# Optimization experiments

Hardware: AMD Instinct MI355X
Metric: run time of the kernel (lower is better)

The kernel has to match this reference:

```python
import jax, jax.numpy as jnp
import numpy as np
from jax import lax

K = 3
STRIDE = 1
PAD = 1
DIL = 1


def setup_inputs() -> dict:
    key = jax.random.key(0)
    k1, k2, k3 = jax.random.split(key, 3)
    B, C, H, W = 8, 128, 64, 64
    O = 128
    x = jax.random.normal(k1, (B, C, H, W), jnp.float32)
    # offset-predicting conv weights (small init -> small offsets, as in DCN practice)
    w_off = jax.random.normal(k2, (2 * K * K, C, K, K), jnp.float32) * 0.01
    b_off = jnp.zeros((2 * K * K,), jnp.float32)
    # deformable conv weight [O, Cin, K, K], bias=False in the source
    w = jax.random.normal(k3, (O, C, K, K), jnp.float32) * (1.0 / np.sqrt(C * K * K))
    return {"x": x, "w_off": w_off, "b_off": b_off, "w": w}


def _deform_conv(x, offset, w):
    # x: [B,C,H,W]; offset: [B, 2*K*K, Ho, Wo]; w: [O,C,K,K]
    B, C, H, W = x.shape
    Ho, Wo = offset.shape[2], offset.shape[3]
    K2 = K * K
    off = offset.reshape(B, K2, 2, Ho, Wo)
    oy, ox = off[:, :, 0], off[:, :, 1]            # [B,K2,Ho,Wo]
    ky = (jnp.arange(K2) // K).astype(jnp.float32)  # kernel row per tap
    kx = (jnp.arange(K2) % K).astype(jnp.float32)
    base_y = (jnp.arange(Ho) * STRIDE - PAD).astype(jnp.float32)
    base_x = (jnp.arange(Wo) * STRIDE - PAD).astype(jnp.float32)
    py = base_y[None, None, :, None] + ky[None, :, None, None] * DIL + oy
    px = base_x[None, None, None, :] + kx[None, :, None, None] * DIL + ox

    y0 = jnp.floor(py)
    x0 = jnp.floor(px)
    dy = py - y0
    dx = px - x0
    y0i = y0.astype(jnp.int32)
    x0i = x0.astype(jnp.int32)
    bidx = jnp.arange(B)[:, None, None, None]

    def gather(yi, xi):
        valid = (yi >= 0) & (yi < H) & (xi >= 0) & (xi < W)
        yc = jnp.clip(yi, 0, H - 1)
        xc = jnp.clip(xi, 0, W - 1)
        v = x[bidx, :, yc, xc]  # [B,K2,Ho,Wo,C]
        return v * valid[..., None]

    v00 = gather(y0i, x0i)
    v01 = gather(y0i, x0i + 1)
    v10 = gather(y0i + 1, x0i)
    v11 = gather(y0i + 1, x0i + 1)
    samp = (v00 * ((1 - dy) * (1 - dx))[..., None]
            + v01 * ((1 - dy) * dx)[..., None]
            + v10 * (dy * (1 - dx))[..., None]
            + v11 * (dy * dx)[..., None])  # [B,K2,Ho,Wo,C]

    O = w.shape[0]
    return jnp.einsum('bkhwc,ock->bohw', samp, w.reshape(O, C, K2))


def reference(x, w_off, b_off, w):
    # offset conv: standard conv2d, stride/pad/dilation as in __init__
    offset = lax.conv_general_dilated(
        x, w_off, window_strides=(STRIDE, STRIDE),
        padding=[(PAD, PAD), (PAD, PAD)], rhs_dilation=(DIL, DIL))
    offset = offset + b_off[None, :, None, None]
    return _deform_conv(x, offset, w)
```

## Files before the change

### kernel.cpp

```cpp
#include <hip/hip_runtime.h>

#define B_ 8
#define C_ 128
#define H_ 64
#define W_ 64
#define O_ 128
#define F_ 18
#define K2_ 9
#define HW_ 4096
#define CK2_ 1152

#define WR_ 10
#define WC_ 22

typedef __attribute__((ext_vector_type(8))) short short8_t;
typedef __attribute__((ext_vector_type(4))) float f32x4_t;
typedef __attribute__((ext_vector_type(4))) unsigned int uint4_t;

__device__ inline short bf16r(float f) {
  unsigned u = __builtin_bit_cast(unsigned, f);
  u += 0x7FFFu + ((u >> 16) & 1u);
  return (short)(u >> 16);
}
__device__ inline float bflo(unsigned u) {
  return __builtin_bit_cast(float, u << 16);
}
__device__ inline float bfhi(unsigned u) {
  return __builtin_bit_cast(float, u & 0xFFFF0000u);
}

__global__ __launch_bounds__(256) void prep_all_kernel(
    const float* __restrict__ w, const float* __restrict__ w_off,
    const float* __restrict__ x,
    short* __restrict__ w_bt2, short* __restrict__ w_ot2,
    short* __restrict__ x_t) {
  __shared__ float tile[128][65];
  int bid = blockIdx.x, t = threadIdx.x;
  if (bid < 576) {
    int i = bid * 256 + t;
    int kk2 = i & 31, o = (i >> 5) & 127, ks = i >> 12;
    w_bt2[i] = bf16r(w[(o * C_ + (ks & 3) * 32 + kk2) * K2_ + (ks >> 2)]);
  } else if (bid < 720) {
    int i = (bid - 576) * 256 + t;
    int kk2 = i & 31, f = (i >> 5) & 31, ks = i >> 10;
    w_ot2[i] = (f < F_) ? bf16r(w_off[(f * C_ + (ks & 3) * 32 + kk2) * K2_ + (ks >> 2)])
                        : (short)0;
  } else {
    int xb_id = bid - 720;
    int b = xb_id >> 6;
    int p_base = (xb_id & 63) << 6;
    const float* xb = x + ((long)b << 19);
#pragma unroll
    for (int i = 0; i < 32; ++i) {
      int idx = (i << 8) + t;
      int c = idx >> 6, p = idx & 63;
      tile[c][p] = xb[((long)c << 12) + p_base + p];
    }
    __syncthreads();
#pragma unroll
    for (int i = 0; i < 32; ++i) {
      int idx = (i << 8) + t;
      int p = idx >> 7, c = idx & 127;
      x_t[(((long)(b << 12) + p_base + p) << 7) + c] = bf16r(tile[c][p]);
    }
  }
}

__device__ inline short8_t lds16(const short* xs, int pix, int ch) {
  return *(const short8_t*)(xs + (pix << 7) + ((ch ^ (pix & 7)) << 3));
}

__global__ __launch_bounds__(512, 4) void fused_deform_kernel(
    const short* __restrict__ x_t, const short* __restrict__ w_ot2,
    const float* __restrict__ b_off, const short* __restrict__ w_bt2,
    float* __restrict__ out) {
  __shared__ short xs[WR_ * WC_ * 128];

  int tid = threadIdx.x;
  int wv = tid >> 6, lane = tid & 63;
  int row = wv & 3, g = wv >> 2;
  int fr = lane & 15, q = lane >> 4;
  int bid = (int)blockIdx.x;
  int b = bid & 7;
  int tile_id = bid >> 3;
  int ho0 = (tile_id >> 2) << 2;
  int x0b = (tile_id & 3) << 4;
  int ys  = min(max(ho0 - 3, 0), H_ - WR_);
  int xsL = min(max(x0b - 3, 0), W_ - WC_);
  int ye2 = ys + WR_ - 1, xe2 = xsL + WC_ - 1;

  const short* xtb = x_t + ((long)b << 19);

#pragma unroll
  for (int i = 0; i < 7; ++i) {
    int ci = (i << 9) + tid;
    if (ci < WR_ * WC_ * 16) {
      int pix = ci >> 4, ch = ci & 15;
      int yr = pix / WC_, xr = pix - yr * WC_;
      short8_t v = *(const short8_t*)(xtb + ((((ys + yr) << 6) + xsL + xr) << 7) + (ch << 3));
      *(short8_t*)(xs + (pix << 7) + ((ch ^ (pix & 7)) << 3)) = v;
    }
  }
  __syncthreads();

  int ho = ho0 + row;
  int wo = x0b + fr;

  f32x4_t oacc0 = (f32x4_t){0.f, 0.f, 0.f, 0.f};
  f32x4_t oacc1 = (f32x4_t){0.f, 0.f, 0.f, 0.f};
#pragma unroll
  for (int kt = 0; kt < 9; ++kt) {
    int y = ho + kt / 3 - 1, xx = wo + kt % 3 - 1;
    bool ok = (y >= 0) & (y < H_) & (xx >= 0) & (xx < W_);
    int yc = min(max(y, 0), H_ - 1), xc = min(max(xx, 0), W_ - 1);
    int pixA = (yc - ys) * WC_ + (xc - xsL);
#pragma unroll
    for (int s = 0; s < 4; ++s) {
      short8_t bfv = lds16(xs, pixA, (s << 2) + q);
      if (!ok) bfv = (short8_t){0, 0, 0, 0, 0, 0, 0, 0};
      int ks = (kt << 2) + s;
      short8_t a0 = *(const short8_t*)(w_ot2 + (((ks << 5) + fr) << 5) + (q << 3));
      short8_t a1 = *(const short8_t*)(w_ot2 + (((ks << 5) + 16 + fr) << 5) + (q << 3));
      oacc0 = __builtin_amdgcn_mfma_f32_16x16x32_bf16(a0, bfv, oacc0, 0, 0, 0);
      oacc1 = __builtin_amdgcn_mfma_f32_16x16x32_bf16(a1, bfv, oacc1, 0, 0, 0);
    }
  }

  f32x4_t acc[4];
#pragma unroll
  for (int nf = 0; nf < 4; ++nf) acc[nf] = (f32x4_t){0.f, 0.f, 0.f, 0.f};

#pragma unroll
  for (int kt = 0; kt < 9; ++kt) {
    float oy, ox;
    if (kt < 8) {
      oy = __shfl(oacc0[(2 * kt) & 3], fr + ((kt >> 1) << 4), 64);
      ox = __shfl(oacc0[(2 * kt + 1) & 3], fr + ((kt >> 1) << 4), 64);
    } else {
      oy = __shfl(oacc1[0], fr, 64);
      ox = __shfl(oacc1[1], fr, 64);
    }
    oy += b_off[2 * kt];
    ox += b_off[2 * kt + 1];

    float py = (float)(ho + kt / 3 - 1) + oy;
    float px = (float)(wo + kt % 3 - 1) + ox;
    float fy0 = floorf(py), fx0 = floorf(px);
    float dy = py - fy0, dx = px - fx0;
    int y0 = (int)fy0, x0 = (int)fx0;
    int y1 = y0 + 1, x1 = x0 + 1;
    float my0 = (y0 >= 0 && y0 < H_) ? 1.f : 0.f;
    float my1 = (y1 >= 0 && y1 < H_) ? 1.f : 0.f;
    float mx0 = (x0 >= 0 && x0 < W_) ? 1.f : 0.f;
    float mx1 = (x1 >= 0 && x1 < W_) ? 1.f : 0.f;
    float w00 = (1.f - dy) * (1.f - dx) * my0 * mx0;
    float w01 = (1.f - dy) * dx * my0 * mx1;
    float w10 = dy * (1.f - dx) * my1 * mx0;
    float w11 = dy * dx * my1 * mx1;
    int y0c = min(max(y0, 0), H_ - 1), y1c = min(max(y1, 0), H_ - 1);
    int x0c = min(max(x0, 0), W_ - 1), x1c = min(max(x1, 0), W_ - 1);
    int p00 = (y0c - ys) * WC_ + (x0c - xsL), p01 = p00 + (x1c - x0c);
    int p10 = (y1c - ys) * WC_ + (x0c - xsL), p11 = p10 + (x1c - x0c);

    short8_t v00[4], v01[4], v10[4], v11[4];
    unsigned long long bad =
        __ballot((y0c < ys) || (y1c > ye2) || (x0c < xsL) || (x1c > xe2));
    if (bad == 0ULL) {
#pragma unroll
      for (int s = 0; s < 4; ++s) {
        int ch = (s << 2) + q;
        v00[s] = lds16(xs, p00, ch);
        v01[s] = lds16(xs, p01, ch);
        v10[s] = lds16(xs, p10, ch);
        v11[s] = lds16(xs, p11, ch);
      }
    } else {
      const short* g00 = xtb + (((y0c << 6) + x0c) << 7);
      const short* g01 = xtb + (((y0c << 6) + x1c) << 7);
      const short* g10 = xtb + (((y1c << 6) + x0c) << 7);
      const short* g11 = xtb + (((y1c << 6) + x1c) << 7);
#pragma unroll
      for (int s = 0; s < 4; ++s) {
        int c0 = (s << 5) + (q << 3);
        v00[s] = *(const short8_t*)(g00 + c0);
        v01[s] = *(const short8_t*)(g01 + c0);
        v10[s] = *(const short8_t*)(g10 + c0);
        v11[s] = *(const short8_t*)(g11 + c0);
      }
    }

#pragma unroll
    for (int s = 0; s < 4; ++s) {
      uint4_t u00 = __builtin_bit_cast(uint4_t, v00[s]);
      uint4_t u01 = __builtin_bit_cast(uint4_t, v01[s]);
      uint4_t u10 = __builtin_bit_cast(uint4_t, v10[s]);
      uint4_t u11 = __builtin_bit_cast(uint4_t, v11[s]);
      uint4_t sfu;
#pragma unroll
      for (int d = 0; d < 4; ++d) {
        float rlo = w00 * bflo(u00[d]) + w01 * bflo(u01[d]) +
                    w10 * bflo(u10[d]) + w11 * bflo(u11[d]);
        float rhi = w00 * bfhi(u00[d]) + w01 * bfhi(u01[d]) +
                    w10 * bfhi(u10[d]) + w11 * bfhi(u11[d]);
        unsigned p;
        asm("v_cvt_pk_bf16_f32 %0, %1, %2" : "=v"(p) : "v"(rlo), "v"(rhi));
        sfu[d] = p;
      }
      short8_t sf = __builtin_bit_cast(short8_t, sfu);
      int ks = (kt << 2) + s;
      const short* wp = w_bt2 + (((ks << 7) + (g << 6) + fr) << 5) + (q << 3);
#pragma unroll
      for (int nf = 0; nf < 4; ++nf) {
        short8_t wf = *(const short8_t*)(wp + (nf << 9));
        acc[nf] = __builtin_amdgcn_mfma_f32_16x16x32_bf16(wf, sf, acc[nf], 0, 0, 0);
      }
    }
  }

  float* ob = out + ((long)(b * O_) << 12) + (ho << 6) + wo;
#pragma unroll
  for (int nf = 0; nf < 4; ++nf) {
#pragma unroll
    for (int r = 0; r < 4; ++r) {
      ob[(long)(((g << 6) + (nf << 4) + (q << 2) + r)) << 12] = acc[nf][r];
    }
  }
}

extern "C" void kernel_launch(void* const* d_in, const int* in_sizes, int n_in,
                              void* d_out, int out_size, void* d_ws, size_t ws_size,
                              hipStream_t stream) {
  const float* x     = (const float*)d_in[0];
  const float* w_off = (const float*)d_in[1];
  const float* b_off = (const float*)d_in[2];
  const float* w     = (const float*)d_in[3];
  float* out = (float*)d_out;

  short* w_bt2 = (short*)d_ws;
  short* w_ot2 = (short*)((char*)d_ws + 294912);
  short* x_t   = (short*)((char*)d_ws + 294912 + 73728);

  prep_all_kernel<<<1232, 256, 0, stream>>>(w, w_off, x, w_bt2, w_ot2, x_t);
  fused_deform_kernel<<<512, 512, 0, stream>>>(x_t, w_ot2, b_off, w_bt2, out);
}
```

Measured before the change: 68.20 us.

## Split channel reduction across wave groups instead of output channels, reduce via LDS

Before, the two wave groups per row split the output channels and each computed the full offset conv and full bilinear sampling, so both groups duplicated them. Now each group takes half the input channels: it computes a partial offset conv and samples only its half of the channels against all 128 outputs. Partial offsets and partial outputs are summed through shared memory. This removes the duplicated offset-conv and sampling work. In exchange it doubles the accumulator registers, adds extra LDS traffic and barriers, and may lower occupancy.

```diff
diff --git a/kernel.cpp b/kernel.cpp
--- a/kernel.cpp
+++ b/kernel.cpp
@@ -75,6 +75,7 @@
     const float* __restrict__ b_off, const short* __restrict__ w_bt2,
     float* __restrict__ out) {
   __shared__ short xs[WR_ * WC_ * 128];
+  __shared__ float offs[4][16][20];
 
   int tid = threadIdx.x;
   int wv = tid >> 6, lane = tid & 63;
@@ -106,42 +107,61 @@
   int ho = ho0 + row;
   int wo = x0b + fr;
 
-  f32x4_t oacc0 = (f32x4_t){0.f, 0.f, 0.f, 0.f};
-  f32x4_t oacc1 = (f32x4_t){0.f, 0.f, 0.f, 0.f};
+  {
+    f32x4_t oacc0 = (f32x4_t){0.f, 0.f, 0.f, 0.f};
+    f32x4_t oacc1 = (f32x4_t){0.f, 0.f, 0.f, 0.f};
+#pragma unroll
+    for (int kt = 0; kt < 9; ++kt) {
+      int y = ho + kt / 3 - 1, xx = wo + kt % 3 - 1;
+      bool ok = (y >= 0) & (y < H_) & (xx >= 0) & (xx < W_);
+      int yc = min(max(y, 0), H_ - 1), xc = min(max(xx, 0), W_ - 1);
+      int pixA = (yc - ys) * WC_ + (xc - xsL);
+#pragma unroll
+      for (int sh = 0; sh < 2; ++sh) {
+        int s = (g << 1) | sh;
+        short8_t bfv = lds16(xs, pixA, (s << 2) + q);
+        if (!ok) bfv = (short8_t){0, 0, 0, 0, 0, 0, 0, 0};
+        int ks = (kt << 2) + s;
+        short8_t a0 = *(const short8_t*)(w_ot2 + (((ks << 5) + fr) << 5) + (q << 3));
+        short8_t a1 = *(const short8_t*)(w_ot2 + (((ks << 5) + 16 + fr) << 5) + (q << 3));
+        oacc0 = __builtin_amdgcn_mfma_f32_16x16x32_bf16(a0, bfv, oacc0, 0, 0, 0);
+        oacc1 = __builtin_amdgcn_mfma_f32_16x16x32_bf16(a1, bfv, oacc1, 0, 0, 0);
+      }
+    }
+    if (g == 0) {
+#pragma unroll
+      for (int r = 0; r < 4; ++r) {
+        int f0 = (q << 2) + r;
+        offs[row][fr][f0] = oacc0[r] + b_off[f0];
+      }
+      if (q == 0) {
+        offs[row][fr][16] = oacc1[0] + b_off[16];
+        offs[row][fr][17] = oacc1[1] + b_off[17];
+      }
+    }
+    __syncthreads();
+    if (g == 1) {
+#pragma unroll
+      for (int r = 0; r < 4; ++r) {
+        int f0 = (q << 2) + r;
+        offs[row][fr][f0] += oacc0[r];
+      }
+      if (q == 0) {
+        offs[row][fr][16] += oacc1[0];
+        offs[row][fr][17] += oacc1[1];
+      }
+    }
+  }
+  __syncthreads();
+
+  f32x4_t acc[8];
+#pragma unroll
+  for (int nf = 0; nf < 8; ++nf) acc[nf] = (f32x4_t){0.f, 0.f, 0.f, 0.f};
+
 #pragma unroll
   for (int kt = 0; kt < 9; ++kt) {
-    int y = ho + kt / 3 - 1, xx = wo + kt % 3 - 1;
-    bool ok = (y >= 0) & (y < H_) & (xx >= 0) & (xx < W_);
-    int yc = min(max(y, 0), H_ - 1), xc = min(max(xx, 0), W_ - 1);
-    int pixA = (yc - ys) * WC_ + (xc - xsL);
-#pragma unroll
-    for (int s = 0; s < 4; ++s) {
-      short8_t bfv = lds16(xs, pixA, (s << 2) + q);
-      if (!ok) bfv = (short8_t){0, 0, 0, 0, 0, 0, 0, 0};
-      int ks = (kt << 2) + s;
-      short8_t a0 = *(const short8_t*)(w_ot2 + (((ks << 5) + fr) << 5) + (q << 3));
-      short8_t a1 = *(const short8_t*)(w_ot2 + (((ks << 5) + 16 + fr) << 5) + (q << 3));
-      oacc0 = __builtin_amdgcn_mfma_f32_16x16x32_bf16(a0, bfv, oacc0, 0, 0, 0);
-      oacc1 = __builtin_amdgcn_mfma_f32_16x16x32_bf16(a1, bfv, oacc1, 0, 0, 0);
-    }
-  }
-
-  f32x4_t acc[4];
-#pragma unroll
-  for (int nf = 0; nf < 4; ++nf) acc[nf] = (f32x4_t){0.f, 0.f, 0.f, 0.f};
-
-#pragma unroll
-  for (int kt = 0; kt < 9; ++kt) {
-    float oy, ox;
-    if (kt < 8) {
-      oy = __shfl(oacc0[(2 * kt) & 3], fr + ((kt >> 1) << 4), 64);
-      ox = __shfl(oacc0[(2 * kt + 1) & 3], fr + ((kt >> 1) << 4), 64);
-    } else {
-      oy = __shfl(oacc1[0], fr, 64);
-      ox = __shfl(oacc1[1], fr, 64);
-    }
-    oy += b_off[2 * kt];
-    ox += b_off[2 * kt + 1];
+    float oy = offs[row][fr][2 * kt];
+    float ox = offs[row][fr][2 * kt + 1];
 
     float py = (float)(ho + kt / 3 - 1) + oy;
     float px = (float)(wo + kt % 3 - 1) + ox;
@@ -162,17 +182,18 @@
     int p00 = (y0c - ys) * WC_ + (x0c - xsL), p01 = p00 + (x1c - x0c);
     int p10 = (y1c - ys) * WC_ + (x0c - xsL), p11 = p10 + (x1c - x0c);
 
-    short8_t v00[4], v01[4], v10[4], v11[4];
+    short8_t v00[2], v01[2], v10[2], v11[2];
     unsigned long long bad =
         __ballot((y0c < ys) || (y1c > ye2) || (x0c < xsL) || (x1c > xe2));
     if (bad == 0ULL) {
 #pragma unroll
-      for (int s = 0; s < 4; ++s) {
+      for (int sh = 0; sh < 2; ++sh) {
+        int s = (g << 1) | sh;
         int ch = (s << 2) + q;
-        v00[s] = lds16(xs, p00, ch);
-        v01[s] = lds16(xs, p01, ch);
-        v10[s] = lds16(xs, p10, ch);
-        v11[s] = lds16(xs, p11, ch);
+        v00[sh] = lds16(xs, p00, ch);
+        v01[sh] = lds16(xs, p01, ch);
+        v10[sh] = lds16(xs, p10, ch);
+        v11[sh] = lds16(xs, p11, ch);
       }
     } else {
       const short* g00 = xtb + (((y0c << 6) + x0c) << 7);
@@ -180,21 +201,23 @@
       const short* g10 = xtb + (((y1c << 6) + x0c) << 7);
       const short* g11 = xtb + (((y1c << 6) + x1c) << 7);
 #pragma unroll
-      for (int s = 0; s < 4; ++s) {
+      for (int sh = 0; sh < 2; ++sh) {
+        int s = (g << 1) | sh;
         int c0 = (s << 5) + (q << 3);
-        v00[s] = *(const short8_t*)(g00 + c0);
-        v01[s] = *(const short8_t*)(g01 + c0);
-        v10[s] = *(const short8_t*)(g10 + c0);
-        v11[s] = *(const short8_t*)(g11 + c0);
-      }
-    }
-
-#pragma unroll
-    for (int s = 0; s < 4; ++s) {
-      uint4_t u00 = __builtin_bit_cast(uint4_t, v00[s]);
-      uint4_t u01 = __builtin_bit_cast(uint4_t, v01[s]);
-      uint4_t u10 = __builtin_bit_cast(uint4_t, v10[s]);
-      uint4_t u11 = __builtin_bit_cast(uint4_t, v11[s]);
+        v00[sh] = *(const short8_t*)(g00 + c0);
+        v01[sh] = *(const short8_t*)(g01 + c0);
+        v10[sh] = *(const short8_t*)(g10 + c0);
+        v11[sh] = *(const short8_t*)(g11 + c0);
+      }
+    }
+
+#pragma unroll
+    for (int sh = 0; sh < 2; ++sh) {
+      int s = (g << 1) | sh;
+      uint4_t u00 = __builtin_bit_cast(uint4_t, v00[sh]);
+      uint4_t u01 = __builtin_bit_cast(uint4_t, v01[sh]);
+      uint4_t u10 = __builtin_bit_cast(uint4_t, v10[sh]);
+      uint4_t u11 = __builtin_bit_cast(uint4_t, v11[sh]);
       uint4_t sfu;
 #pragma unroll
       for (int d = 0; d < 4; ++d) {
@@ -208,21 +231,33 @@
       }
       short8_t sf = __builtin_bit_cast(short8_t, sfu);
       int ks = (kt << 2) + s;
-      const short* wp = w_bt2 + (((ks << 7) + (g << 6) + fr) << 5) + (q << 3);
-#pragma unroll
-      for (int nf = 0; nf < 4; ++nf) {
+      const short* wp = w_bt2 + (((ks << 7) + fr) << 5) + (q << 3);
+#pragma unroll
+      for (int nf = 0; nf < 8; ++nf) {
         short8_t wf = *(const short8_t*)(wp + (nf << 9));
         acc[nf] = __builtin_amdgcn_mfma_f32_16x16x32_bf16(wf, sf, acc[nf], 0, 0, 0);
       }
     }
   }
 
-  float* ob = out + ((long)(b * O_) << 12) + (ho << 6) + wo;
-#pragma unroll
-  for (int nf = 0; nf < 4; ++nf) {
-#pragma unroll
-    for (int r = 0; r < 4; ++r) {
-      ob[(long)(((g << 6) + (nf << 4) + (q << 2) + r)) << 12] = acc[nf][r];
+  __syncthreads();
+  float* red = (float*)xs;
+  if (g == 1) {
+#pragma unroll
+    for (int nf = 0; nf < 8; ++nf) {
+      *(f32x4_t*)&red[(row * 16 + fr) * 136 + (nf << 4) + (q << 2)] = acc[nf];
+    }
+  }
+  __syncthreads();
+  if (g == 0) {
+    float* ob = out + ((long)(b * O_) << 12) + (ho << 6) + wo;
+#pragma unroll
+    for (int nf = 0; nf < 8; ++nf) {
+      f32x4_t other = *(const f32x4_t*)&red[(row * 16 + fr) * 136 + (nf << 4) + (q << 2)];
+#pragma unroll
+      for (int r = 0; r < 4; ++r) {
+        ob[(long)((nf << 4) + (q << 2) + r) << 12] = acc[nf][r] + other[r];
+      }
     }
   }
 }
```

Measured after the change: 60.07 us. 11.9% less time.
